# Kernel tuning notes

Hardware: AMD Instinct MI355X
Metric: run time of the kernel (lower is better)

## Reference

```python
import jax, jax.numpy as jnp
import numpy as np

IMG = 224          # image_size
FMAP = (56, 56)    # feature_map_dims (AdaptiveAvgPool2d((56,56)))
K_REWEIGHT = 3     # self.n_reweight
BLUR_RADIUS = 4    # KNNGaussianBlur(4): kernel 9, sigma 4


def _cdist(a, b):
    # Euclidean pairwise distance, [Na, D] x [Nb, D] -> [Na, Nb]
    a2 = jnp.sum(a * a, axis=1, keepdims=True)            # [Na,1]
    b2 = jnp.sum(b * b, axis=1, keepdims=True).T          # [1,Nb]
    d2 = a2 + b2 - 2.0 * (a @ b.T)
    return jnp.sqrt(jnp.maximum(d2, 0.0))


def _gaussian_blur(x):
    # x: [1,1,H,W]; torchvision GaussianBlur(kernel=9, sigma=4), reflect pad
    r, sigma = BLUR_RADIUS, float(BLUR_RADIUS)
    t = jnp.arange(2 * r + 1, dtype=x.dtype) - r
    g = jnp.exp(-(t * t) / (2.0 * sigma * sigma))
    g = g / jnp.sum(g)
    k2d = jnp.outer(g, g)[None, None]                     # [1,1,9,9]
    xp = jnp.pad(x, ((0, 0), (0, 0), (r, r), (r, r)), mode='reflect')
    return jax.lax.conv_general_dilated(
        xp, k2d, window_strides=(1, 1), padding='VALID',
        dimension_numbers=('NCHW', 'OIHW', 'NCHW'))


def setup_inputs() -> dict:
    key = jax.random.key(0)
    k1, k2 = jax.random.split(key)
    patch = jax.random.normal(k1, (FMAP[0] * FMAP[1], 768), dtype=jnp.float32)
    patch_lib = jax.random.normal(k2, (16384, 768), dtype=jnp.float32)
    mean = jnp.zeros((), dtype=jnp.float32)
    std = jnp.ones((), dtype=jnp.float32)
    return {"patch": patch, "patch_lib": patch_lib, "mean": mean, "std": std}


def reference(patch, patch_lib, mean, std):
    # normalization (method_name != 'Point_MAE' branch)
    p = (patch - mean) / std                               # [N, D]

    dist = _cdist(p, patch_lib)                            # [N, Nlib]
    min_val = jnp.min(dist, axis=1)                        # [N]
    min_idx = jnp.argmin(dist, axis=1)                     # [N]
    s_idx = jnp.argmax(min_val)
    s_star = jnp.max(min_val)

    m_test = p[s_idx]                                      # [D]
    m_star = patch_lib[min_idx[s_idx]]                     # [D]

    # distances of m_star to whole bank, k smallest
    w_dist = jnp.sqrt(jnp.maximum(
        jnp.sum((patch_lib - m_star) ** 2, axis=1), 0.0))  # [Nlib]
    _, nn_idx = jax.lax.top_k(-w_dist, K_REWEIGHT)         # smallest k
    m_star_knn = jnp.linalg.norm(
        m_test[None, :] - patch_lib[nn_idx[1:]], axis=1)   # [k-1]

    D_sqrt = jnp.sqrt(jnp.asarray(patch.shape[1], dtype=p.dtype))
    w = 1.0 - jnp.exp(s_star / D_sqrt) / jnp.sum(jnp.exp(m_star_knn / D_sqrt))
    s = w * s_star

    s_map = min_val.reshape(1, 1, *FMAP)
    s_map = jax.image.resize(s_map, (1, 1, IMG, IMG), method='bilinear')
    s_map = _gaussian_blur(s_map)
    return s, s_map
```

## Files before the change

kernel.cpp:

```cpp
#include <hip/hip_runtime.h>
#include <hip/hip_bf16.h>
#include <stdint.h>

#define N_PATCH 3136
#define N_PATCH_PAD 3200
#define N_LIB   16384
#define DIM     768
#define IMGSZ   224
#define FM      56

#define BK 32
#define KT 24
#define MT 25
#define NTILES 128

#define TAILB 64
#define D2_MARGIN 8.0f
#define COLLECT_MARGIN 0.015f

typedef __bf16 bf16_t;
typedef __bf16 bf16x8 __attribute__((ext_vector_type(8)));
typedef __bf16 bf16x4_v __attribute__((ext_vector_type(4)));
typedef float  f32x4  __attribute__((ext_vector_type(4)));

#define FLT_MAX_ 3.402823466e+38f

struct Scal {
  unsigned long long approx_max_pack;
  unsigned long long cand_pack[64];
  int cand[64];
  int cand_count;
  int bar[4];
};

__device__ __forceinline__ float wave_reduce_sum(float v) {
#pragma unroll
  for (int s = 32; s > 0; s >>= 1) v += __shfl_xor(v, s, 64);
  return v;
}

__device__ __forceinline__ unsigned long long shfl_xor_u64(unsigned long long v, int mask) {
  unsigned lo = (unsigned)v, hi = (unsigned)(v >> 32);
  lo = __shfl_xor(lo, mask, 64);
  hi = __shfl_xor(hi, mask, 64);
  return ((unsigned long long)hi << 32) | lo;
}

__device__ __forceinline__ void async16(const bf16_t* g, bf16_t* l) {
  __builtin_amdgcn_global_load_lds(
      (const __attribute__((address_space(1))) unsigned int*)g,
      (__attribute__((address_space(3))) unsigned int*)l, 16, 0, 0);
}

__device__ __forceinline__ void grid_bar(int* ctr, int nb) {
  __syncthreads();
  if (threadIdx.x == 0) {
    __threadfence();
    atomicAdd(ctr, 1);
    while (atomicAdd(ctr, 0) < nb) __builtin_amdgcn_s_sleep(8);
    __threadfence();
  }
  __syncthreads();
}

__device__ __forceinline__ float bf16u_to_f(unsigned short u) {
  return __uint_as_float(((unsigned)u) << 16);
}

__global__ void prep_kernel(const float* __restrict__ patch, const float* __restrict__ lib,
                            const float* __restrict__ meanp, const float* __restrict__ stdp,
                            bf16_t* __restrict__ pb, bf16_t* __restrict__ lb,
                            float* __restrict__ a2, float* __restrict__ b2, Scal* sc) {
  int t = threadIdx.x;
  int lane = t & 63;
  if (blockIdx.x == 0) {
    if (t < 64) sc->cand_pack[t] = ~0ULL;
    if (t == 64) { sc->approx_max_pack = 0ULL; sc->cand_count = 0; }
    if (t >= 65 && t < 69) sc->bar[t - 65] = 0;
  }
  if (blockIdx.x < N_PATCH / 4) {
    int row = blockIdx.x * 4 + (t >> 6);
    float mu = meanp[0], sd = stdp[0];
    float acc = 0.f;
#pragma unroll
    for (int k = 0; k < 3; k++) {
      float4 v = ((const float4*)(patch + (size_t)row * DIM))[lane + 64 * k];
      v.x = (v.x - mu) / sd; v.y = (v.y - mu) / sd;
      v.z = (v.z - mu) / sd; v.w = (v.w - mu) / sd;
      bf16x4_v o = {(__bf16)v.x, (__bf16)v.y, (__bf16)v.z, (__bf16)v.w};
      *(bf16x4_v*)(pb + (size_t)row * DIM + (lane + 64 * k) * 4) = o;
      acc += v.x*v.x + v.y*v.y + v.z*v.z + v.w*v.w;
    }
    acc = wave_reduce_sum(acc);
    if (lane == 0) a2[row] = acc;
  } else {
    int row = (blockIdx.x - N_PATCH / 4) * 4 + (t >> 6);
    float acc = 0.f;
#pragma unroll
    for (int k = 0; k < 3; k++) {
      float4 v = ((const float4*)(lib + (size_t)row * DIM))[lane + 64 * k];
      bf16x4_v o = {(__bf16)v.x, (__bf16)v.y, (__bf16)v.z, (__bf16)v.w};
      *(bf16x4_v*)(lb + (size_t)row * DIM + (lane + 64 * k) * 4) = o;
      acc += v.x*v.x + v.y*v.y + v.z*v.z + v.w*v.w;
    }
    acc = wave_reduce_sum(acc);
    if (lane == 0) b2[row] = acc;
  }
}

__global__ __launch_bounds__(256, 3)
void gemm_min_kernel(const bf16_t* __restrict__ pb, const bf16_t* __restrict__ lb,
                     const float* __restrict__ a2, const float* __restrict__ b2,
                     float* __restrict__ part) {
  __shared__ __align__(16) bf16_t As[2][128 * BK];
  __shared__ __align__(16) bf16_t Bs[2][128 * BK];
  __shared__ unsigned smin[128];

  const int t = threadIdx.x;
  const int wave = t >> 6;
  const int lane = t & 63;
  const int l15 = lane & 15;
  const int quad = lane >> 4;
  const int wm = (wave >> 1) * 64;
  const int wn = (wave & 1) * 64;

  const int lid = blockIdx.x;
  const int xcd = lid & 7;
  const int slot = lid >> 3;
  const int ntile = xcd + 8 * (slot / MT);
  const int mtile = slot % MT;
  const int m0 = mtile * 128;
  const int n0 = ntile * 128;

  int ra0 = m0 + (t >> 2);       if (ra0 > N_PATCH - 1) ra0 = N_PATCH - 1;
  int ra1 = m0 + 64 + (t >> 2);  if (ra1 > N_PATCH - 1) ra1 = N_PATCH - 1;
  const bf16_t* gA0 = pb + (size_t)ra0 * DIM + (t & 3) * 8;
  const bf16_t* gA1 = pb + (size_t)ra1 * DIM + (t & 3) * 8;
  const bf16_t* gB0 = lb + (size_t)(n0 + (t >> 2)) * DIM + (t & 3) * 8;
  const bf16_t* gB1 = gB0 + (size_t)64 * DIM;

  if (t < 128) smin[t] = 0xffffffffu;

  {
    bf16_t* la = &As[0][0];
    bf16_t* lb_ = &Bs[0][0];
    async16(gA0, la + t * 8);
    async16(gA1, la + 2048 + t * 8);
    async16(gB0, lb_ + t * 8);
    async16(gB1, lb_ + 2048 + t * 8);
  }
  __syncthreads();

  f32x4 acc[4][4];
#pragma unroll
  for (int mi = 0; mi < 4; mi++)
#pragma unroll
    for (int ni = 0; ni < 4; ni++) { f32x4 z = {0.f,0.f,0.f,0.f}; acc[mi][ni] = z; }

  for (int k = 0; k < KT; ++k) {
    const int cur = k & 1;
    if (k + 1 < KT) {
      const int nxt = cur ^ 1;
      const size_t ko = (size_t)(k + 1) * BK;
      bf16_t* la = &As[nxt][0];
      bf16_t* lb_ = &Bs[nxt][0];
      async16(gA0 + ko, la + t * 8);
      async16(gA1 + ko, la + 2048 + t * 8);
      async16(gB0 + ko, lb_ + t * 8);
      async16(gB1 + ko, lb_ + 2048 + t * 8);
    }

    bf16x8 afr[4], bfr[4];
#pragma unroll
    for (int mi = 0; mi < 4; mi++)
      afr[mi] = *(const bf16x8*)(&As[cur][(wm + mi * 16 + l15) * BK + quad * 8]);
#pragma unroll
    for (int ni = 0; ni < 4; ni++)
      bfr[ni] = *(const bf16x8*)(&Bs[cur][(wn + ni * 16 + l15) * BK + quad * 8]);
#pragma unroll
    for (int mi = 0; mi < 4; mi++)
#pragma unroll
      for (int ni = 0; ni < 4; ni++)
        acc[mi][ni] = __builtin_amdgcn_mfma_f32_16x16x32_bf16(afr[mi], bfr[ni],
                                                              acc[mi][ni], 0, 0, 0);
    __syncthreads();
  }

  float b2n[4];
#pragma unroll
  for (int ni = 0; ni < 4; ni++) b2n[ni] = b2[n0 + wn + ni * 16 + l15];

#pragma unroll
  for (int mi = 0; mi < 4; mi++) {
#pragma unroll
    for (int r = 0; r < 4; r++) {
      int rloc = wm + mi * 16 + quad * 4 + r;
      int mrow = m0 + rloc;
      float a2v = a2[mrow < N_PATCH ? mrow : (N_PATCH - 1)];
      float best = a2v + b2n[0] - 2.0f * acc[mi][0][r];
#pragma unroll
      for (int ni = 1; ni < 4; ni++)
        best = fminf(best, a2v + b2n[ni] - 2.0f * acc[mi][ni][r]);
      best = fmaxf(best, 0.0f);
#pragma unroll
      for (int s = 1; s < 16; s <<= 1)
        best = fminf(best, __shfl_xor(best, s, 64));
      if (l15 == 0) atomicMin(&smin[rloc], __float_as_uint(best));
    }
  }
  __syncthreads();
  if (t < 128) part[(size_t)ntile * N_PATCH_PAD + m0 + t] = __uint_as_float(smin[t]);
}

__device__ __forceinline__ void wave_pick(const Scal* sc, int cnt, int lane,
                                          int* srow, float* sstar, int* ms) {
  unsigned long long pk = 0ULL;
  int rowv = 0, msv = 0;
  if (lane < cnt) {
    unsigned long long cp = sc->cand_pack[lane];
    rowv = sc->cand[lane];
    msv = (int)(cp & 0xffffffffu);
    pk = (cp & 0xffffffff00000000ULL) | (unsigned)(0xffffffffu - (unsigned)rowv);
  }
  unsigned long long m = pk;
#pragma unroll
  for (int s = 1; s < 64; s <<= 1) {
    unsigned long long o = shfl_xor_u64(m, s);
    if (o > m) m = o;
  }
  unsigned long long mask = __ballot(pk == m && lane < cnt);
  int wl = (int)(__ffsll((long long)mask) - 1);
  *srow = __shfl(rowv, wl, 64);
  *ms   = __shfl(msv, wl, 64);
  *sstar = sqrtf(__uint_as_float((unsigned)(m >> 32)));
}

__global__ __launch_bounds__(256, 2)
void tail_kernel(const float* __restrict__ part, float* __restrict__ min_val,
                 const float* __restrict__ patch, const float* __restrict__ lib,
                 const bf16_t* __restrict__ lb,
                 const float* __restrict__ meanp, const float* __restrict__ stdp,
                 Scal* __restrict__ sc, float* __restrict__ wdist2,
                 float* __restrict__ out0, float* __restrict__ outmap) {
  __shared__ union {
    unsigned long long sl[768];
    float rs[40 * 40];
  } sm;
  __shared__ int s_cnt;

  const int t = threadIdx.x;
  const int b = blockIdx.x;
  const int wave = t >> 6, lane = t & 63;

  {
    int row = b * 256 + t;
    if (row < N_PATCH) {
      float m = FLT_MAX_;
#pragma unroll 8
      for (int nt = 0; nt < NTILES; nt++)
        m = fminf(m, part[(size_t)nt * N_PATCH_PAD + row]);
      float v = sqrtf(m);
      min_val[row] = v;
      unsigned long long mp = (((unsigned long long)__float_as_uint(v)) << 32) |
                              (unsigned)(0xffffffffu - (unsigned)row);
      atomicMax(&sc->approx_max_pack, mp);
    }
  }
  grid_bar(&sc->bar[0], TAILB);

  if (b == 0) {
    unsigned long long mp = atomicMax(&sc->approx_max_pack, 0ULL);
    float amax = __uint_as_float((unsigned)(mp >> 32));
    int arow = (int)(0xffffffffu - (unsigned)(mp & 0xffffffffu));
    if (t == 0) { sc->cand[0] = arow; sc->cand_count = 1; }
    __syncthreads();
    for (int i = t; i < N_PATCH; i += 256) {
      if (i != arow && min_val[i] >= amax - COLLECT_MARGIN) {
        int p = atomicAdd(&sc->cand_count, 1);
        if (p < 64) sc->cand[p] = i;
      }
    }
  }
  grid_bar(&sc->bar[1], TAILB);

  if (t == 0) s_cnt = atomicAdd(&sc->cand_count, 0);
  __syncthreads();
  int cnt = s_cnt; if (cnt > 64) cnt = 64;

  {
    float mu = meanp[0], sd = stdp[0];
    for (int c = 0; c < cnt; c++) {
      int row = sc->cand[c];
      float mv = min_val[row];
      float bmin = mv * mv;
      bool loaded = false;
      float4 pv[3];
#pragma unroll
      for (int tt = 0; tt < 2; tt++) {
        int nt = 2 * b + tt;
        float pmin = part[(size_t)nt * N_PATCH_PAD + row];
        if (pmin <= bmin + D2_MARGIN) {
          if (!loaded) {
#pragma unroll
            for (int k = 0; k < 3; k++) {
              float4 v = ((const float4*)(patch + (size_t)row * DIM))[lane + 64 * k];
              v.x = (v.x - mu) / sd; v.y = (v.y - mu) / sd;
              v.z = (v.z - mu) / sd; v.w = (v.w - mu) / sd;
              pv[k] = v;
            }
            loaded = true;
          }
          unsigned long long best = ~0ULL;
          int jb = nt * 128 + wave * 32;
          for (int rr = 0; rr < 32; rr++) {
            int j = jb + rr;
            const float4* pl = (const float4*)(lib + (size_t)j * DIM);
            float acc = 0.f;
#pragma unroll
            for (int k = 0; k < 3; k++) {
              float4 l = pl[lane + 64 * k];
              float dx = pv[k].x - l.x, dy = pv[k].y - l.y;
              float dz = pv[k].z - l.z, dw = pv[k].w - l.w;
              acc += dx*dx + dy*dy + dz*dz + dw*dw;
            }
            acc = wave_reduce_sum(acc);
            unsigned long long pk = (((unsigned long long)__float_as_uint(acc)) << 32) | (unsigned)j;
            if (pk < best) best = pk;
          }
          if (lane == 0) atomicMin(&sc->cand_pack[c], best);
        }
      }
    }
  }
  grid_bar(&sc->bar[2], TAILB);

  {
    int srow_, ms; float ss_;
    wave_pick(sc, cnt, lane, &srow_, &ss_, &ms);
    float pm[12];
    const ushort4* pms = (const ushort4*)(lb + (size_t)ms * DIM);
#pragma unroll
    for (int k = 0; k < 3; k++) {
      ushort4 u = pms[lane + 64 * k];
      pm[k*4+0] = bf16u_to_f(u.x); pm[k*4+1] = bf16u_to_f(u.y);
      pm[k*4+2] = bf16u_to_f(u.z); pm[k*4+3] = bf16u_to_f(u.w);
    }
    int jbase = b * 256 + wave * 64;
    for (int rr = 0; rr < 64; rr += 2) {
      int j0 = jbase + rr, j1 = j0 + 1;
      const ushort4* r0 = (const ushort4*)(lb + (size_t)j0 * DIM);
      const ushort4* r1 = (const ushort4*)(lb + (size_t)j1 * DIM);
      float a0 = 0.f, a1 = 0.f;
#pragma unroll
      for (int k = 0; k < 3; k++) {
        ushort4 u0 = r0[lane + 64 * k];
        ushort4 u1 = r1[lane + 64 * k];
        float d;
        d = bf16u_to_f(u0.x) - pm[k*4+0]; a0 += d * d;
        d = bf16u_to_f(u0.y) - pm[k*4+1]; a0 += d * d;
        d = bf16u_to_f(u0.z) - pm[k*4+2]; a0 += d * d;
        d = bf16u_to_f(u0.w) - pm[k*4+3]; a0 += d * d;
        d = bf16u_to_f(u1.x) - pm[k*4+0]; a1 += d * d;
        d = bf16u_to_f(u1.y) - pm[k*4+1]; a1 += d * d;
        d = bf16u_to_f(u1.z) - pm[k*4+2]; a1 += d * d;
        d = bf16u_to_f(u1.w) - pm[k*4+3]; a1 += d * d;
      }
      a0 = wave_reduce_sum(a0);
      a1 = wave_reduce_sum(a1);
      if (lane == 0) { wdist2[j0] = a0; wdist2[j1] = a1; }
    }
  }
  grid_bar(&sc->bar[3], TAILB);

  if (b == 0) {
    unsigned long long b0 = ~0ULL, b1 = ~0ULL, b2 = ~0ULL;
    for (int j = t; j < N_LIB; j += 256) {
      unsigned long long pk = (((unsigned long long)__float_as_uint(wdist2[j])) << 32) | (unsigned)j;
      if (pk < b0)      { b2 = b1; b1 = b0; b0 = pk; }
      else if (pk < b1) { b2 = b1; b1 = pk; }
      else if (pk < b2) { b2 = pk; }
    }
    sm.sl[t * 3 + 0] = b0; sm.sl[t * 3 + 1] = b1; sm.sl[t * 3 + 2] = b2;
    __syncthreads();
    if (t >= 64) return;

    unsigned long long c0 = ~0ULL, c1 = ~0ULL, c2 = ~0ULL;
#pragma unroll
    for (int e = 0; e < 12; e++) {
      unsigned long long pk = sm.sl[t * 12 + e];
      if (pk < c0)      { c2 = c1; c1 = c0; c0 = pk; }
      else if (pk < c1) { c2 = c1; c1 = pk; }
      else if (pk < c2) { c2 = pk; }
    }
    unsigned long long res1 = 0, res2 = 0;
#pragma unroll
    for (int r = 0; r < 3; r++) {
      unsigned long long m = c0;
#pragma unroll
      for (int s = 1; s < 64; s <<= 1) {
        unsigned long long o = shfl_xor_u64(m, s);
        if (o < m) m = o;
      }
      if (r == 1) res1 = m;
      if (r == 2) res2 = m;
      if (c0 == m) { c0 = c1; c1 = c2; c2 = ~0ULL; }
    }
    int nA = (int)(res1 & 0xffffffffu);
    int nB = (int)(res2 & 0xffffffffu);

    int srow, ms2; float sstar;
    wave_pick(sc, cnt, t, &srow, &sstar, &ms2);

    float mu = meanp[0], sd = stdp[0];
    float accA = 0.f, accB = 0.f;
#pragma unroll
    for (int k = 0; k < 3; k++) {
      float4 p4 = ((const float4*)(patch + (size_t)srow * DIM))[t + 64 * k];
      float4 a4 = ((const float4*)(lib + (size_t)nA * DIM))[t + 64 * k];
      float4 b4 = ((const float4*)(lib + (size_t)nB * DIM))[t + 64 * k];
      float px = (p4.x - mu) / sd, py = (p4.y - mu) / sd;
      float pz = (p4.z - mu) / sd, pw = (p4.w - mu) / sd;
      float dax = px - a4.x, day = py - a4.y, daz = pz - a4.z, daw = pw - a4.w;
      float dbx = px - b4.x, dby = py - b4.y, dbz = pz - b4.z, dbw = pw - b4.w;
      accA += dax*dax + day*day + daz*daz + daw*daw;
      accB += dbx*dbx + dby*dby + dbz*dbz + dbw*dbw;
    }
    accA = wave_reduce_sum(accA);
    accB = wave_reduce_sum(accB);
    if (t == 0) {
      float dsq = sqrtf((float)DIM);
      float d1 = sqrtf(accA), d2v = sqrtf(accB);
      float w = 1.0f - expf(sstar / dsq) / (expf(d1 / dsq) + expf(d2v / dsq));
      out0[0] = w * sstar;
    }
    return;
  }

  if (b > 49) return;
  {
    int tile = b - 1;
    int bx = tile % 7, by = tile / 7;
    int ox0 = bx * 32, oy0 = by * 32;

    for (int i = t; i < 1600; i += 256) {
      int ly = i / 40, lx = i % 40;
      int gy = oy0 - 4 + ly; gy = gy < 0 ? 0 : (gy > 223 ? 223 : gy);
      int gx = ox0 - 4 + lx; gx = gx < 0 ? 0 : (gx > 223 ? 223 : gx);
      float sy = fminf(fmaxf(0.25f * gy - 0.375f, 0.0f), 55.0f);
      float sx = fminf(fmaxf(0.25f * gx - 0.375f, 0.0f), 55.0f);
      int y0 = (int)sy; if (y0 > 54) y0 = 54;
      int x0 = (int)sx; if (x0 > 54) x0 = 54;
      float fy = sy - y0, fx = sx - x0;
      float v00 = min_val[y0*FM + x0],     v01 = min_val[y0*FM + x0 + 1];
      float v10 = min_val[(y0+1)*FM + x0], v11 = min_val[(y0+1)*FM + x0 + 1];
      float a = v00 + fx * (v01 - v00);
      float bb = v10 + fx * (v11 - v10);
      sm.rs[i] = a + fy * (bb - a);
    }
    __syncthreads();

    float g[9]; float gs = 0.f;
#pragma unroll
    for (int i = 0; i < 9; i++) { float tt = (float)(i - 4); g[i] = expf(-(tt*tt)/32.0f); gs += g[i]; }
#pragma unroll
    for (int i = 0; i < 9; i++) g[i] /= gs;

    for (int p = t; p < 1024; p += 256) {
      int y = oy0 + p / 32, x = ox0 + (p & 31);
      float acc = 0.f;
#pragma unroll
      for (int dy = 0; dy < 9; dy++) {
        int yy = y + dy - 4;
        yy = yy < 0 ? -yy : (yy > IMGSZ - 1 ? 2*(IMGSZ-1) - yy : yy);
        int lyy = yy - (oy0 - 4);
        float ra = 0.f;
#pragma unroll
        for (int dx = 0; dx < 9; dx++) {
          int xx = x + dx - 4;
          xx = xx < 0 ? -xx : (xx > IMGSZ - 1 ? 2*(IMGSZ-1) - xx : xx);
          ra += g[dx] * sm.rs[lyy * 40 + (xx - (ox0 - 4))];
        }
        acc += g[dy] * ra;
      }
      outmap[y * IMGSZ + x] = acc;
    }
  }
}

extern "C" void kernel_launch(void* const* d_in, const int* in_sizes, int n_in,
                              void* d_out, int out_size, void* d_ws, size_t ws_size,
                              hipStream_t stream) {
  const float* patch = (const float*)d_in[0];
  const float* lib   = (const float*)d_in[1];
  const float* meanp = (const float*)d_in[2];
  const float* stdp  = (const float*)d_in[3];
  float* out = (float*)d_out;

  char* ws = (char*)d_ws;
  size_t off = 0;
  auto alloc = [&](size_t bytes) -> void* {
    void* p = ws + off;
    off = (off + bytes + 255) & ~(size_t)255;
    return p;
  };
  bf16_t* pb      = (bf16_t*)alloc((size_t)N_PATCH * DIM * sizeof(bf16_t));
  bf16_t* lb      = (bf16_t*)alloc((size_t)N_LIB * DIM * sizeof(bf16_t));
  float* a2       = (float*)alloc(N_PATCH * sizeof(float));
  float* b2       = (float*)alloc(N_LIB * sizeof(float));
  float* part     = (float*)alloc((size_t)N_PATCH_PAD * NTILES * sizeof(float));
  float* min_val  = (float*)alloc(N_PATCH * sizeof(float));
  float* wdist2   = (float*)alloc(N_LIB * sizeof(float));
  Scal*  sc       = (Scal*)alloc(sizeof(Scal));

  prep_kernel<<<N_PATCH / 4 + N_LIB / 4, 256, 0, stream>>>(patch, lib, meanp, stdp,
                                                           pb, lb, a2, b2, sc);
  gemm_min_kernel<<<MT * NTILES, 256, 0, stream>>>(pb, lb, a2, b2, part);
  tail_kernel<<<TAILB, 256, 0, stream>>>(part, min_val, patch, lib, lb, meanp, stdp,
                                         sc, wdist2, out, out + 1);
}
```

Measured before the change: 320.9 us.

## Remove a grid barrier by collecting candidates redundantly per block, batch prep rows

Result: slower. 328.6 us (+2.4%).

```diff
diff --git a/kernel.cpp b/kernel.cpp
--- a/kernel.cpp
+++ b/kernel.cpp
@@ -28,9 +28,7 @@
 struct Scal {
   unsigned long long approx_max_pack;
   unsigned long long cand_pack[64];
-  int cand[64];
-  int cand_count;
-  int bar[4];
+  int bar[3];
 };
 
 __device__ __forceinline__ float wave_reduce_sum(float v) {
@@ -57,7 +55,7 @@
   if (threadIdx.x == 0) {
     __threadfence();
     atomicAdd(ctr, 1);
-    while (atomicAdd(ctr, 0) < nb) __builtin_amdgcn_s_sleep(8);
+    while (atomicAdd(ctr, 0) < nb) __builtin_amdgcn_s_sleep(1);
     __threadfence();
   }
   __syncthreads();
@@ -72,39 +70,41 @@
                             bf16_t* __restrict__ pb, bf16_t* __restrict__ lb,
                             float* __restrict__ a2, float* __restrict__ b2, Scal* sc) {
   int t = threadIdx.x;
-  int lane = t & 63;
+  int wave = t >> 6, lane = t & 63;
   if (blockIdx.x == 0) {
     if (t < 64) sc->cand_pack[t] = ~0ULL;
-    if (t == 64) { sc->approx_max_pack = 0ULL; sc->cand_count = 0; }
-    if (t >= 65 && t < 69) sc->bar[t - 65] = 0;
-  }
-  if (blockIdx.x < N_PATCH / 4) {
-    int row = blockIdx.x * 4 + (t >> 6);
-    float mu = meanp[0], sd = stdp[0];
-    float acc = 0.f;
-#pragma unroll
-    for (int k = 0; k < 3; k++) {
-      float4 v = ((const float4*)(patch + (size_t)row * DIM))[lane + 64 * k];
-      v.x = (v.x - mu) / sd; v.y = (v.y - mu) / sd;
-      v.z = (v.z - mu) / sd; v.w = (v.w - mu) / sd;
-      bf16x4_v o = {(__bf16)v.x, (__bf16)v.y, (__bf16)v.z, (__bf16)v.w};
-      *(bf16x4_v*)(pb + (size_t)row * DIM + (lane + 64 * k) * 4) = o;
-      acc += v.x*v.x + v.y*v.y + v.z*v.z + v.w*v.w;
-    }
-    acc = wave_reduce_sum(acc);
-    if (lane == 0) a2[row] = acc;
-  } else {
-    int row = (blockIdx.x - N_PATCH / 4) * 4 + (t >> 6);
-    float acc = 0.f;
-#pragma unroll
-    for (int k = 0; k < 3; k++) {
-      float4 v = ((const float4*)(lib + (size_t)row * DIM))[lane + 64 * k];
-      bf16x4_v o = {(__bf16)v.x, (__bf16)v.y, (__bf16)v.z, (__bf16)v.w};
-      *(bf16x4_v*)(lb + (size_t)row * DIM + (lane + 64 * k) * 4) = o;
-      acc += v.x*v.x + v.y*v.y + v.z*v.z + v.w*v.w;
-    }
-    acc = wave_reduce_sum(acc);
-    if (lane == 0) b2[row] = acc;
+    if (t == 64) sc->approx_max_pack = 0ULL;
+    if (t >= 65 && t < 68) sc->bar[t - 65] = 0;
+  }
+  const int nbp = N_PATCH / 16;
+  bool isp = blockIdx.x < nbp;
+  int row0 = (isp ? blockIdx.x : blockIdx.x - nbp) * 16 + wave * 4;
+  const float* src = isp ? patch : lib;
+  bf16_t* dst = isp ? pb : lb;
+  float* nrm = isp ? a2 : b2;
+  float mu = isp ? meanp[0] : 0.f;
+  float inv_sd = isp ? (1.0f / stdp[0]) : 1.0f;
+
+  float acc[4] = {0.f, 0.f, 0.f, 0.f};
+#pragma unroll
+  for (int k = 0; k < 3; k++) {
+    float4 v[4];
+#pragma unroll
+    for (int r = 0; r < 4; r++)
+      v[r] = ((const float4*)(src + (size_t)(row0 + r) * DIM))[lane + 64 * k];
+#pragma unroll
+    for (int r = 0; r < 4; r++) {
+      float x = (v[r].x - mu) * inv_sd, y = (v[r].y - mu) * inv_sd;
+      float z = (v[r].z - mu) * inv_sd, w = (v[r].w - mu) * inv_sd;
+      bf16x4_v o = {(__bf16)x, (__bf16)y, (__bf16)z, (__bf16)w};
+      *(bf16x4_v*)(dst + (size_t)(row0 + r) * DIM + (lane + 64 * k) * 4) = o;
+      acc[r] += x * x + y * y + z * z + w * w;
+    }
+  }
+#pragma unroll
+  for (int r = 0; r < 4; r++) {
+    float s = wave_reduce_sum(acc[r]);
+    if (lane == 0) nrm[row0 + r] = s;
   }
 }
 
@@ -212,13 +212,13 @@
   if (t < 128) part[(size_t)ntile * N_PATCH_PAD + m0 + t] = __uint_as_float(smin[t]);
 }
 
-__device__ __forceinline__ void wave_pick(const Scal* sc, int cnt, int lane,
-                                          int* srow, float* sstar, int* ms) {
+__device__ __forceinline__ void wave_pick(const Scal* sc, const int* cand_l, int cnt,
+                                          int lane, int* srow, float* sstar, int* ms) {
   unsigned long long pk = 0ULL;
   int rowv = 0, msv = 0;
   if (lane < cnt) {
     unsigned long long cp = sc->cand_pack[lane];
-    rowv = sc->cand[lane];
+    rowv = cand_l[lane];
     msv = (int)(cp & 0xffffffffu);
     pk = (cp & 0xffffffff00000000ULL) | (unsigned)(0xffffffffu - (unsigned)rowv);
   }
@@ -246,7 +246,10 @@
     unsigned long long sl[768];
     float rs[40 * 40];
   } sm;
-  __shared__ int s_cnt;
+  __shared__ int cand_l[64];
+  __shared__ int wsum[4];
+  __shared__ int ccount;
+  __shared__ unsigned trig[4];
 
   const int t = threadIdx.x;
   const int b = blockIdx.x;
@@ -268,75 +271,86 @@
   }
   grid_bar(&sc->bar[0], TAILB);
 
-  if (b == 0) {
+  {
     unsigned long long mp = atomicMax(&sc->approx_max_pack, 0ULL);
     float amax = __uint_as_float((unsigned)(mp >> 32));
     int arow = (int)(0xffffffffu - (unsigned)(mp & 0xffffffffu));
-    if (t == 0) { sc->cand[0] = arow; sc->cand_count = 1; }
+    if (t == 0) { cand_l[0] = arow; ccount = 1; }
     __syncthreads();
-    for (int i = t; i < N_PATCH; i += 256) {
-      if (i != arow && min_val[i] >= amax - COLLECT_MARGIN) {
-        int p = atomicAdd(&sc->cand_count, 1);
-        if (p < 64) sc->cand[p] = i;
+    for (int base = 0; base < N_PATCH; base += 256) {
+      int i = base + t;
+      bool hit = (i < N_PATCH) && (i != arow) && (min_val[i] >= amax - COLLECT_MARGIN);
+      unsigned long long mask = __ballot(hit);
+      if (lane == 0) wsum[wave] = __popcll(mask);
+      __syncthreads();
+      int off = ccount;
+      for (int w = 0; w < wave; w++) off += wsum[w];
+      int myoff = off + (int)__popcll(mask & ((1ULL << lane) - 1ULL));
+      if (hit && myoff < 64) cand_l[myoff] = i;
+      __syncthreads();
+      if (t == 0) {
+        int tot = wsum[0] + wsum[1] + wsum[2] + wsum[3];
+        ccount = min(64, ccount + tot);
       }
+      __syncthreads();
+    }
+  }
+  int cnt = ccount;
+
+  {
+    if (t < 4) trig[t] = 0;
+    __syncthreads();
+    if (t < 2 * cnt) {
+      int c = t >> 1, tt = t & 1;
+      int row = cand_l[c];
+      float mv = min_val[row];
+      float pmin = part[(size_t)(2 * b + tt) * N_PATCH_PAD + row];
+      if (pmin <= mv * mv + D2_MARGIN) atomicOr(&trig[t >> 5], 1u << (t & 31));
+    }
+    __syncthreads();
+    float mu = meanp[0], sd = stdp[0];
+#pragma unroll 1
+    for (int i = 0; i < 4; i++) {
+      unsigned m = trig[i];
+      while (m) {
+        int bit = __ffs(m) - 1; m &= m - 1;
+        int pair = i * 32 + bit;
+        int c = pair >> 1, tt = pair & 1;
+        int row = cand_l[c];
+        float4 pv[3];
+#pragma unroll
+        for (int k = 0; k < 3; k++) {
+          float4 v = ((const float4*)(patch + (size_t)row * DIM))[lane + 64 * k];
+          v.x = (v.x - mu) / sd; v.y = (v.y - mu) / sd;
+          v.z = (v.z - mu) / sd; v.w = (v.w - mu) / sd;
+          pv[k] = v;
+        }
+        unsigned long long best = ~0ULL;
+        int jb = (2 * b + tt) * 128 + wave * 32;
+        for (int rr = 0; rr < 32; rr++) {
+          int j = jb + rr;
+          const float4* pl = (const float4*)(lib + (size_t)j * DIM);
+          float acc = 0.f;
+#pragma unroll
+          for (int k = 0; k < 3; k++) {
+            float4 l = pl[lane + 64 * k];
+            float dx = pv[k].x - l.x, dy = pv[k].y - l.y;
+            float dz = pv[k].z - l.z, dw = pv[k].w - l.w;
+            acc += dx*dx + dy*dy + dz*dz + dw*dw;
+          }
+          acc = wave_reduce_sum(acc);
+          unsigned long long pk = (((unsigned long long)__float_as_uint(acc)) << 32) | (unsigned)j;
+          if (pk < best) best = pk;
+        }
+        if (lane == 0) atomicMin(&sc->cand_pack[c], best);
+      }
     }
   }
   grid_bar(&sc->bar[1], TAILB);
-
-  if (t == 0) s_cnt = atomicAdd(&sc->cand_count, 0);
-  __syncthreads();
-  int cnt = s_cnt; if (cnt > 64) cnt = 64;
-
-  {
-    float mu = meanp[0], sd = stdp[0];
-    for (int c = 0; c < cnt; c++) {
-      int row = sc->cand[c];
-      float mv = min_val[row];
-      float bmin = mv * mv;
-      bool loaded = false;
-      float4 pv[3];
-#pragma unroll
-      for (int tt = 0; tt < 2; tt++) {
-        int nt = 2 * b + tt;
-        float pmin = part[(size_t)nt * N_PATCH_PAD + row];
-        if (pmin <= bmin + D2_MARGIN) {
-          if (!loaded) {
-#pragma unroll
-            for (int k = 0; k < 3; k++) {
-              float4 v = ((const float4*)(patch + (size_t)row * DIM))[lane + 64 * k];
-              v.x = (v.x - mu) / sd; v.y = (v.y - mu) / sd;
-              v.z = (v.z - mu) / sd; v.w = (v.w - mu) / sd;
-              pv[k] = v;
-            }
-            loaded = true;
-          }
-          unsigned long long best = ~0ULL;
-          int jb = nt * 128 + wave * 32;
-          for (int rr = 0; rr < 32; rr++) {
-            int j = jb + rr;
-            const float4* pl = (const float4*)(lib + (size_t)j * DIM);
-            float acc = 0.f;
-#pragma unroll
-            for (int k = 0; k < 3; k++) {
-              float4 l = pl[lane + 64 * k];
-              float dx = pv[k].x - l.x, dy = pv[k].y - l.y;
-              float dz = pv[k].z - l.z, dw = pv[k].w - l.w;
-              acc += dx*dx + dy*dy + dz*dz + dw*dw;
-            }
-            acc = wave_reduce_sum(acc);
-            unsigned long long pk = (((unsigned long long)__float_as_uint(acc)) << 32) | (unsigned)j;
-            if (pk < best) best = pk;
-          }
-          if (lane == 0) atomicMin(&sc->cand_pack[c], best);
-        }
-      }
-    }
-  }
-  grid_bar(&sc->bar[2], TAILB);
 
   {
     int srow_, ms; float ss_;
-    wave_pick(sc, cnt, lane, &srow_, &ss_, &ms);
+    wave_pick(sc, cand_l, cnt, lane, &srow_, &ss_, &ms);
     float pm[12];
     const ushort4* pms = (const ushort4*)(lb + (size_t)ms * DIM);
 #pragma unroll
@@ -346,31 +360,31 @@
       pm[k*4+2] = bf16u_to_f(u.z); pm[k*4+3] = bf16u_to_f(u.w);
     }
     int jbase = b * 256 + wave * 64;
-    for (int rr = 0; rr < 64; rr += 2) {
-      int j0 = jbase + rr, j1 = j0 + 1;
-      const ushort4* r0 = (const ushort4*)(lb + (size_t)j0 * DIM);
-      const ushort4* r1 = (const ushort4*)(lb + (size_t)j1 * DIM);
-      float a0 = 0.f, a1 = 0.f;
+    for (int rr = 0; rr < 64; rr += 4) {
+      float a[4] = {0.f, 0.f, 0.f, 0.f};
 #pragma unroll
       for (int k = 0; k < 3; k++) {
-        ushort4 u0 = r0[lane + 64 * k];
-        ushort4 u1 = r1[lane + 64 * k];
-        float d;
-        d = bf16u_to_f(u0.x) - pm[k*4+0]; a0 += d * d;
-        d = bf16u_to_f(u0.y) - pm[k*4+1]; a0 += d * d;
-        d = bf16u_to_f(u0.z) - pm[k*4+2]; a0 += d * d;
-        d = bf16u_to_f(u0.w) - pm[k*4+3]; a0 += d * d;
-        d = bf16u_to_f(u1.x) - pm[k*4+0]; a1 += d * d;
-        d = bf16u_to_f(u1.y) - pm[k*4+1]; a1 += d * d;
-        d = bf16u_to_f(u1.z) - pm[k*4+2]; a1 += d * d;
-        d = bf16u_to_f(u1.w) - pm[k*4+3]; a1 += d * d;
+        ushort4 u[4];
+#pragma unroll
+        for (int q = 0; q < 4; q++)
+          u[q] = ((const ushort4*)(lb + (size_t)(jbase + rr + q) * DIM))[lane + 64 * k];
+#pragma unroll
+        for (int q = 0; q < 4; q++) {
+          float d;
+          d = bf16u_to_f(u[q].x) - pm[k*4+0]; a[q] += d * d;
+          d = bf16u_to_f(u[q].y) - pm[k*4+1]; a[q] += d * d;
+          d = bf16u_to_f(u[q].z) - pm[k*4+2]; a[q] += d * d;
+          d = bf16u_to_f(u[q].w) - pm[k*4+3]; a[q] += d * d;
+        }
       }
-      a0 = wave_reduce_sum(a0);
-      a1 = wave_reduce_sum(a1);
-      if (lane == 0) { wdist2[j0] = a0; wdist2[j1] = a1; }
-    }
-  }
-  grid_bar(&sc->bar[3], TAILB);
+#pragma unroll
+      for (int q = 0; q < 4; q++) {
+        float s = wave_reduce_sum(a[q]);
+        if (lane == 0) wdist2[jbase + rr + q] = s;
+      }
+    }
+  }
+  grid_bar(&sc->bar[2], TAILB);
 
   if (b == 0) {
     unsigned long long b0 = ~0ULL, b1 = ~0ULL, b2 = ~0ULL;
@@ -409,7 +423,7 @@
     int nB = (int)(res2 & 0xffffffffu);
 
     int srow, ms2; float sstar;
-    wave_pick(sc, cnt, t, &srow, &sstar, &ms2);
+    wave_pick(sc, cand_l, cnt, t, &srow, &sstar, &ms2);
 
     float mu = meanp[0], sd = stdp[0];
     float accA = 0.f, accB = 0.f;
@@ -512,8 +526,8 @@
   float* wdist2   = (float*)alloc(N_LIB * sizeof(float));
   Scal*  sc       = (Scal*)alloc(sizeof(Scal));
 
-  prep_kernel<<<N_PATCH / 4 + N_LIB / 4, 256, 0, stream>>>(patch, lib, meanp, stdp,
-                                                           pb, lb, a2, b2, sc);
+  prep_kernel<<<N_PATCH / 16 + N_LIB / 16, 256, 0, stream>>>(patch, lib, meanp, stdp,
+                                                             pb, lb, a2, b2, sc);
   gemm_min_kernel<<<MT * NTILES, 256, 0, stream>>>(pb, lb, a2, b2, part);
   tail_kernel<<<TAILB, 256, 0, stream>>>(part, min_val, patch, lib, lb, meanp, stdp,
                                          sc, wdist2, out, out + 1);
```
